# Optimization experiments

Measured on AMD Instinct MI355X. Metric: run time of the kernel, lower is better.

## Reference

```python
import jax, jax.numpy as jnp
import numpy as np

# dims: NL layers, D=d_model, DI=expand*D, F=d_ff, V=vocab, L=S*C seq, R=dt_rank, N=d_state, K=d_conv
NL, D, DI, F, V, L, R, N, K = 2, 256, 512, 1024, 1024, 1024, 16, 16, 4
B, S, C = 2, 128, 8
EPS = 1e-5


def silu(x):
    return x * jax.nn.sigmoid(x)


def batchnorm(x, g, b):  # x: [B,L,D], normalize over (B,L) per channel (training-mode BatchNorm1d)
    m = x.mean((0, 1))
    v = x.var((0, 1))
    return (x - m) * jax.lax.rsqrt(v + EPS) * g + b


def layernorm(x, g, b):
    m = x.mean(-1, keepdims=True)
    v = x.var(-1, keepdims=True)
    return (x - m) * jax.lax.rsqrt(v + EPS) * g + b


def mamba(x, Win, cw, cb, Wx, Wdt, bdt, A_log, Dsk, Wout, bout):
    # x: [B,L,D] -> [B,L,D]; standard Mamba block with selective scan
    Bsz, Lseq, _ = x.shape
    xz = x @ Win                      # [B,L,2*DI]
    xi, z = jnp.split(xz, 2, axis=-1)
    # depthwise causal conv1d, width K
    xp = jnp.pad(xi, ((0, 0), (K - 1, 0), (0, 0)))
    xc = cb + sum(xp[:, k:k + Lseq, :] * cw[:, k] for k in range(K))
    xc = silu(xc)                     # [B,L,DI]
    xdb = xc @ Wx                     # [B,L,R+2N]
    delta = jax.nn.softplus(xdb[..., :R] @ Wdt + bdt)   # [B,L,DI]
    Bm = xdb[..., R:R + N]            # [B,L,N]
    Cm = xdb[..., R + N:]             # [B,L,N]
    A = -jnp.exp(A_log)               # [DI,N]
    dA = jnp.exp(delta[..., None] * A)                       # [B,L,DI,N]
    dBx = delta[..., None] * Bm[:, :, None, :] * xc[..., None]  # [B,L,DI,N]

    def step(h, inp):
        dA_t, dBx_t, C_t = inp
        h = h * dA_t + dBx_t          # [B,DI,N]
        y = jnp.einsum('bdn,bn->bd', h, C_t)
        return h, y

    h0 = jnp.zeros((Bsz, DI, N), x.dtype)
    _, ys = jax.lax.scan(step, h0, (dA.transpose(1, 0, 2, 3), dBx.transpose(1, 0, 2, 3), Cm.transpose(1, 0, 2)))
    y = ys.transpose(1, 0, 2) + Dsk * xc
    y = y * silu(z)
    return y @ Wout + bout


def _forward(input_ids, emb, pos, Win, conv_w, conv_b, Wx, Wdt, bdt, A_log, Dskip, Wout, bout,
             bn_g, bn_b, ln_g, ln_b, ff_w1, ff_b1, ff_w2, ff_b2, final_w, final_b):
    Bsz, Ssz, Csz = input_ids.shape
    Lseq = Ssz * Csz
    # Encoder: token embedding (scaled) + learned positions, flattened to [B, S*C, D]
    x = emb[input_ids].reshape(Bsz, Lseq, D) * jnp.sqrt(jnp.float32(D)) + pos[:Lseq]
    for i in range(NL):
        f = mamba(x, Win[i, 0], conv_w[i, 0], conv_b[i, 0], Wx[i, 0], Wdt[i, 0], bdt[i, 0],
                  A_log[i, 0], Dskip[i, 0], Wout[i, 0], bout[i, 0])
        f = batchnorm(f, bn_g[i, 0], bn_b[i, 0])
        bk = mamba(x[:, ::-1], Win[i, 1], conv_w[i, 1], conv_b[i, 1], Wx[i, 1], Wdt[i, 1], bdt[i, 1],
                   A_log[i, 1], Dskip[i, 1], Wout[i, 1], bout[i, 1])
        bk = batchnorm(bk, bn_g[i, 1], bn_b[i, 1])[:, ::-1]
        f = layernorm(x + f, ln_g[i, 0], ln_b[i, 0])
        bk = layernorm(x + bk, ln_g[i, 1], ln_b[i, 1])
        out = f + bk
        out = jax.nn.relu(out @ ff_w1[i] + ff_b1[i]) @ ff_w2[i] + ff_b2[i]
        out = batchnorm(out, bn_g[i, 2], bn_b[i, 2])
        x = out + x
    return x.reshape(Bsz, Ssz, Csz, D) @ final_w + final_b   # [B,S,C,V]


def setup_inputs() -> dict:
    key = jax.random.key(0)
    ks = list(jax.random.split(key, 16))
    kit = iter(ks)
    rn = lambda shape, s=0.02: jax.random.normal(next(kit), shape, jnp.float32) * s
    inp = {
        'input_ids': jax.random.randint(next(kit), (B, S, C), 0, V),
        'emb': rn((V, D)), 'pos': rn((L, D)),
        'Win': rn((NL, 2, D, 2 * DI)),
        'conv_w': rn((NL, 2, DI, K), 0.1), 'conv_b': jnp.zeros((NL, 2, DI)),
        'Wx': rn((NL, 2, DI, R + 2 * N)),
        'Wdt': rn((NL, 2, R, DI)), 'bdt': jnp.full((NL, 2, DI), -4.0),
        'A_log': jnp.broadcast_to(jnp.log(jnp.arange(1, N + 1, dtype=jnp.float32)), (NL, 2, DI, N)) + 0.0,
        'Dskip': jnp.ones((NL, 2, DI)),
        'Wout': rn((NL, 2, DI, D)), 'bout': jnp.zeros((NL, 2, D)),
        'bn_g': jnp.ones((NL, 3, D)), 'bn_b': jnp.zeros((NL, 3, D)),
        'ln_g': jnp.ones((NL, 2, D)), 'ln_b': jnp.zeros((NL, 2, D)),
        'ff_w1': rn((NL, D, F)), 'ff_b1': jnp.zeros((NL, F)),
        'ff_w2': rn((NL, F, D)), 'ff_b2': jnp.zeros((NL, D)),
        'final_w': rn((D, V)), 'final_b': jnp.zeros((V,)),
    }
    return inp


def reference(input_ids, emb, pos, Win, conv_w, conv_b, Wx, Wdt, bdt, A_log, Dskip, Wout, bout,
              bn_g, bn_b, ln_g, ln_b, ff_w1, ff_b1, ff_w2, ff_b2, final_w, final_b):
    return _forward(input_ids, emb, pos, Win, conv_w, conv_b, Wx, Wdt, bdt, A_log, Dskip, Wout, bout,
                    bn_g, bn_b, ln_g, ln_b, ff_w1, ff_b1, ff_w2, ff_b2, final_w, final_b)
```

## Files before the change

### kernel.cpp

```cpp
#include <hip/hip_runtime.h>

#define NL 2
#define DMODEL 256
#define DI 512
#define FF 1024
#define VV 1024
#define LSEQ 1024
#define RR 16
#define NN 16
#define KCONV 4
#define BTOK 2048
#define EPS 1e-5f

using short8 = __attribute__((ext_vector_type(8))) short;
using float4v = __attribute__((ext_vector_type(4))) float;
typedef unsigned short u16;

__device__ inline float bf2f(u16 u) {
    union { unsigned u; float f; } x; x.u = (unsigned)u << 16; return x.f;
}
__device__ inline u16 f2bf(float f) {
    union { float f; unsigned u; } x; x.f = f;
    unsigned r = x.u + 0x7fffu + ((x.u >> 16) & 1u);
    return (u16)(r >> 16);
}

#if __has_builtin(__builtin_amdgcn_exp2f)
#define EXP2(x) __builtin_amdgcn_exp2f(x)
#else
#define EXP2(x) exp2f(x)
#endif

struct TMat { const float* src; u16* dst; int rows, cols, tile0, tilecols; };
struct TTable { TMat m[24]; int nmat; };

__global__ __launch_bounds__(256) void transpose_kernel(TTable tt) {
    __shared__ u16 tile[32][33];
    int bx = blockIdx.x;
    int j = 0;
    for (int k = 1; k < tt.nmat; ++k) if (bx >= tt.m[k].tile0) j = k;
    TMat mm = tt.m[j];
    int lt = bx - mm.tile0;
    int r0 = (lt / mm.tilecols) * 32, c0 = (lt % mm.tilecols) * 32;
    int tx = threadIdx.x & 31, ty = threadIdx.x >> 5;
    #pragma unroll
    for (int k = 0; k < 4; ++k) {
        int r = r0 + ty + k * 8, c = c0 + tx;
        tile[ty + k * 8][tx] = (r < mm.rows && c < mm.cols) ? f2bf(mm.src[(size_t)r * mm.cols + c]) : (u16)0;
    }
    __syncthreads();
    #pragma unroll
    for (int k = 0; k < 4; ++k) {
        int c = c0 + ty + k * 8, r = r0 + tx;
        if (c < mm.cols && r < mm.rows) mm.dst[(size_t)c * mm.rows + r] = tile[tx][ty + k * 8];
    }
}

__global__ __launch_bounds__(256) void gemm_kernel(
    const u16* __restrict__ A0, int lda, unsigned long long sA,
    const u16* __restrict__ B0, int ldb, unsigned long long sB,
    const float* __restrict__ bias0, unsigned long long sBias,
    void* __restrict__ C0, int ldc, unsigned long long sC,
    int M, int N, int K, int act, int outfp)
{
    const u16* A = A0 + (size_t)blockIdx.z * sA;
    const u16* Bt = B0 + (size_t)blockIdx.z * sB;
    const float* bias = bias0 ? (bias0 + (size_t)blockIdx.z * sBias) : nullptr;

    int tid = threadIdx.x;
    int wv = tid >> 6, lane = tid & 63;
    int row0 = blockIdx.y * 64 + (wv >> 1) * 32;
    int col0 = blockIdx.x * 64 + (wv & 1) * 32;
    int mi = lane & 15, kq = lane >> 4;

    float4v acc[2][2];
    #pragma unroll
    for (int a = 0; a < 2; ++a)
        #pragma unroll
        for (int b = 0; b < 2; ++b) acc[a][b] = (float4v){0.f, 0.f, 0.f, 0.f};
    const short8 zer = {0, 0, 0, 0, 0, 0, 0, 0};

    for (int kk = 0; kk < K; kk += 32) {
        int k = kk + kq * 8;
        bool kv = (k < K);
        short8 af[2], bf[2];
        #pragma unroll
        for (int rt = 0; rt < 2; ++rt) {
            int r = row0 + rt * 16 + mi;
            af[rt] = kv ? *(const short8*)(A + (size_t)r * lda + k) : zer;
        }
        #pragma unroll
        for (int ct = 0; ct < 2; ++ct) {
            int n = col0 + ct * 16 + mi;
            bf[ct] = (kv && n < N) ? *(const short8*)(Bt + (size_t)n * ldb + k) : zer;
        }
        #pragma unroll
        for (int rt = 0; rt < 2; ++rt)
            #pragma unroll
            for (int ct = 0; ct < 2; ++ct)
                acc[rt][ct] = __builtin_amdgcn_mfma_f32_16x16x32_bf16(af[rt], bf[ct], acc[rt][ct], 0, 0, 0);
    }

    #pragma unroll
    for (int rt = 0; rt < 2; ++rt)
        #pragma unroll
        for (int ct = 0; ct < 2; ++ct) {
            int n = col0 + ct * 16 + mi;
            if (n >= N) continue;
            float bv = bias ? bias[n] : 0.f;
            #pragma unroll
            for (int r = 0; r < 4; ++r) {
                int m = row0 + rt * 16 + kq * 4 + r;
                float v = acc[rt][ct][r] + bv;
                if (act == 1) v = fmaxf(v, 0.f);
                if (outfp)
                    ((float*)C0)[(size_t)blockIdx.z * sC + (size_t)m * ldc + n] = v;
                else
                    ((u16*)C0)[(size_t)blockIdx.z * sC + (size_t)m * ldc + n] = f2bf(v);
            }
        }
}

__global__ __launch_bounds__(256) void delta_fused_kernel(
    const u16* __restrict__ xdb, const u16* __restrict__ wdtT,
    const float* __restrict__ bdt, const u16* __restrict__ xc,
    u16* __restrict__ deltaT, u16* __restrict__ uT, int layer)
{
    int z = blockIdx.z;
    const u16* A = xdb + (size_t)z * BTOK * 48;
    const u16* Bt = wdtT + (size_t)z * 512 * 16;
    const float* bias = bdt + (size_t)z * 512;

    int tid = threadIdx.x;
    int wv = tid >> 6, lane = tid & 63;
    int row0 = blockIdx.y * 64 + (wv >> 1) * 32;
    int col0 = blockIdx.x * 64 + (wv & 1) * 32;
    int mi = lane & 15, kq = lane >> 4;

    float4v acc[2][2];
    #pragma unroll
    for (int a = 0; a < 2; ++a)
        #pragma unroll
        for (int b = 0; b < 2; ++b) acc[a][b] = (float4v){0.f, 0.f, 0.f, 0.f};
    const short8 zer = {0, 0, 0, 0, 0, 0, 0, 0};

    int k = kq * 8;
    bool kv = (k < 16);
    short8 af[2], bf[2];
    #pragma unroll
    for (int rt = 0; rt < 2; ++rt) {
        int r = row0 + rt * 16 + mi;
        af[rt] = kv ? *(const short8*)(A + (size_t)r * 48 + k) : zer;
    }
    #pragma unroll
    for (int ct = 0; ct < 2; ++ct) {
        int n = col0 + ct * 16 + mi;
        bf[ct] = kv ? *(const short8*)(Bt + (size_t)n * 16 + k) : zer;
    }
    #pragma unroll
    for (int rt = 0; rt < 2; ++rt)
        #pragma unroll
        for (int ct = 0; ct < 2; ++ct)
            acc[rt][ct] = __builtin_amdgcn_mfma_f32_16x16x32_bf16(af[rt], bf[ct], acc[rt][ct], 0, 0, 0);

    #pragma unroll
    for (int rt = 0; rt < 2; ++rt)
        #pragma unroll
        for (int ct = 0; ct < 2; ++ct) {
            int n = col0 + ct * 16 + mi;
            float bv = bias[n];
            #pragma unroll
            for (int r = 0; r < 4; ++r) {
                int m = row0 + rt * 16 + kq * 4 + r;
                float v = acc[rt][ct][r] + bv;
                v = (v > 20.f) ? v : logf(1.f + __expf(v));
                float xcv = bf2f(xc[((size_t)z * BTOK + m) * DI + n]);
                int b = m >> 10, t = m & 1023;
                size_t off = ((size_t)((z * 2 + b) * DI + n)) * LSEQ + t;
                deltaT[off] = f2bf(v);
                uT[off] = f2bf(v * xcv);
            }
        }
}

__global__ __launch_bounds__(256) void bct_kernel(
    const u16* __restrict__ xdb, u16* __restrict__ bcT)
{
    __shared__ u16 tile[32][34];
    int slab = blockIdx.y;
    int t0 = blockIdx.x * 32;
    int tx = threadIdx.x & 31, ty = threadIdx.x >> 5;
    #pragma unroll
    for (int k = 0; k < 4; ++k) {
        int t = t0 + ty + k * 8;
        tile[tx][ty + k * 8] = xdb[(size_t)(slab * 1024 + t) * 48 + 16 + tx];
    }
    __syncthreads();
    #pragma unroll
    for (int k = 0; k < 4; ++k) {
        int col = ty + k * 8;
        bcT[((size_t)(slab * 32 + col)) * LSEQ + t0 + tx] = tile[col][tx];
    }
}

__global__ __launch_bounds__(256) void embed_kernel(
    const int* __restrict__ ids, const float* __restrict__ emb,
    const float* __restrict__ pos, u16* __restrict__ x)
{
    int tok = blockIdx.x, d = threadIdx.x;
    int id = ids[tok];
    float v = emb[(size_t)id * DMODEL + d] * 16.0f + pos[(size_t)(tok & (LSEQ - 1)) * DMODEL + d];
    x[(size_t)tok * DMODEL + d] = f2bf(v);
}

__global__ __launch_bounds__(256) void conv_kernel(
    const u16* __restrict__ xz, const float* __restrict__ conv_w,
    const float* __restrict__ conv_b, u16* __restrict__ xc, int layer)
{
    unsigned g = blockIdx.x * 256u + threadIdx.x;
    int d = g & 511;
    int t = (g >> 9) & 1023;
    int b = (g >> 19) & 1;
    int dir = g >> 20;
    int wbase = ((layer * 2 + dir) * DI + d);
    float acc = conv_b[wbase];
    int colbase = dir * 1024 + d;
    #pragma unroll
    for (int k = 0; k < KCONV; ++k) {
        int ts = dir ? (t + 3 - k) : (t - 3 + k);
        if (ts >= 0 && ts < LSEQ)
            acc += conv_w[wbase * KCONV + k] * bf2f(xz[(size_t)((b << 10) + ts) * 2048 + colbase]);
    }
    float v = acc / (1.f + __expf(-acc));
    xc[(size_t)(((dir * 2 + b) << 10) + t) * DI + d] = f2bf(v);
}

template<int DIR>
__device__ __forceinline__ void scan_body(
    const u16* __restrict__ deltaT, const u16* __restrict__ uT,
    const u16* __restrict__ bcT, const float* __restrict__ A_log,
    u16* __restrict__ pT, int layer, int slab,
    float* Ps, float* Qs)
{
    const int c = threadIdx.x;
    const int d = blockIdx.x;

    float a2[16];
    const float* al = A_log + (size_t)(((layer * 2 + DIR) * DI + d) * NN);
    #pragma unroll
    for (int n = 0; n < 16; ++n) a2[n] = -__expf(al[n]) * 1.44269504f;

    const size_t tb = ((size_t)(slab * DI + d)) * LSEQ;
    const size_t bcb = (size_t)slab * 32 * LSEQ;
    const int T0 = DIR ? (1016 - 8 * c) : (8 * c);

    short8 dlv = *(const short8*)(deltaT + tb + T0);
    short8 uvv = *(const short8*)(uT + tb + T0);
    float dls[8], uvs[8];
    #pragma unroll
    for (int s = 0; s < 8; ++s) {
        const int idx = DIR ? 7 - s : s;
        dls[s] = bf2f((u16)dlv[idx]);
        uvs[s] = bf2f((u16)uvv[idx]);
    }

    const int base = c * 17;
    #pragma unroll
    for (int n = 0; n < 16; ++n) {
        short8 B8 = *(const short8*)(bcT + bcb + (size_t)n * LSEQ + T0);
        float P = 1.f, Q = 0.f;
        #pragma unroll
        for (int s = 0; s < 8; ++s) {
            const int idx = DIR ? 7 - s : s;
            float dA = EXP2(dls[s] * a2[n]);
            Q = Q * dA + uvs[s] * bf2f((u16)B8[idx]);
            P *= dA;
        }
        Ps[base + n] = P;
        Qs[base + n] = Q;
    }
    __syncthreads();

    for (int off = 1; off < 128; off <<= 1) {
        float np[16], nq[16];
        const bool act = (c >= off);
        if (act) {
            const int nb = (c - off) * 17;
            #pragma unroll
            for (int n = 0; n < 16; ++n) { np[n] = Ps[nb + n]; nq[n] = Qs[nb + n]; }
        }
        __syncthreads();
        if (act) {
            #pragma unroll
            for (int n = 0; n < 16; ++n) {
                float p = Ps[base + n], q = Qs[base + n];
                Qs[base + n] = fmaf(p, nq[n], q);
                Ps[base + n] = p * np[n];
            }
        }
        __syncthreads();
    }

    float pacc[8];
    #pragma unroll
    for (int s = 0; s < 8; ++s) pacc[s] = 0.f;
    const int hb = (c - 1) * 17;
    #pragma unroll
    for (int n = 0; n < 16; ++n) {
        short8 B8 = *(const short8*)(bcT + bcb + (size_t)n * LSEQ + T0);
        short8 C8 = *(const short8*)(bcT + bcb + (size_t)(16 + n) * LSEQ + T0);
        float h = (c == 0) ? 0.f : Qs[hb + n];
        #pragma unroll
        for (int s = 0; s < 8; ++s) {
            const int idx = DIR ? 7 - s : s;
            float dA = EXP2(dls[s] * a2[n]);
            h = h * dA + uvs[s] * bf2f((u16)B8[idx]);
            pacc[s] = fmaf(h, bf2f((u16)C8[idx]), pacc[s]);
        }
    }
    short8 pk;
    #pragma unroll
    for (int s = 0; s < 8; ++s) {
        const int idx = DIR ? 7 - s : s;
        pk[idx] = (short)f2bf(pacc[s]);
    }
    *(short8*)(pT + tb + T0) = pk;
}

__global__ __launch_bounds__(128) void scan_kernel(
    const u16* __restrict__ deltaT, const u16* __restrict__ uT,
    const u16* __restrict__ bcT, const float* __restrict__ A_log,
    u16* __restrict__ pT, int layer)
{
    __shared__ float Ps[128 * 17], Qs[128 * 17];
    int slab = blockIdx.y;
    if (slab >> 1)
        scan_body<1>(deltaT, uT, bcT, A_log, pT, layer, slab, Ps, Qs);
    else
        scan_body<0>(deltaT, uT, bcT, A_log, pT, layer, slab, Ps, Qs);
}

__global__ __launch_bounds__(256) void gate_kernel(
    const u16* __restrict__ pT, const u16* __restrict__ xc,
    const u16* __restrict__ xz, const float* __restrict__ Dskip,
    u16* __restrict__ y, int layer)
{
    __shared__ float tile[32][33];
    int z = blockIdx.z, dir = z >> 1, b = z & 1;
    int d0 = blockIdx.x * 32, t0 = blockIdx.y * 32;
    int tx = threadIdx.x & 31, ty = threadIdx.x >> 5;
    #pragma unroll
    for (int k = 0; k < 4; ++k) {
        int d = d0 + ty + k * 8;
        tile[ty + k * 8][tx] = bf2f(pT[((size_t)(z * DI + d)) * LSEQ + t0 + tx]);
    }
    __syncthreads();
    #pragma unroll
    for (int k = 0; k < 4; ++k) {
        int t = t0 + ty + k * 8, d = d0 + tx;
        float p = tile[tx][ty + k * 8];
        float xcv = bf2f(xc[(size_t)((z << 10) + t) * DI + d]);
        float zv = bf2f(xz[(size_t)((b << 10) + t) * 2048 + dir * 1024 + 512 + d]);
        float dsk = Dskip[(layer * 2 + dir) * DI + d];
        float yv = (p + dsk * xcv) * (zv / (1.f + __expf(-zv)));
        y[(size_t)((z << 10) + t) * DI + d] = f2bf(yv);
    }
}

__global__ __launch_bounds__(256) void bnstats_kernel(
    const u16* __restrict__ p0, const u16* __restrict__ p1, float* __restrict__ stats)
{
    int d = blockIdx.x, arr = blockIdx.y, tid = threadIdx.x;
    const u16* p = arr ? p1 : p0;
    float s = 0.f, q = 0.f;
    #pragma unroll
    for (int k = 0; k < 8; ++k) {
        float v = bf2f(p[(size_t)(tid + k * 256) * DMODEL + d]);
        s += v; q += v * v;
    }
    #pragma unroll
    for (int off = 1; off < 64; off <<= 1) { s += __shfl_xor(s, off); q += __shfl_xor(q, off); }
    __shared__ float ss[4], qs[4];
    if ((tid & 63) == 0) { ss[tid >> 6] = s; qs[tid >> 6] = q; }
    __syncthreads();
    if (tid == 0) {
        float S = ss[0] + ss[1] + ss[2] + ss[3];
        float Q2 = qs[0] + qs[1] + qs[2] + qs[3];
        float mean = S * (1.f / 2048.f);
        float var = Q2 * (1.f / 2048.f) - mean * mean;
        stats[(arr * DMODEL + d) * 2] = mean;
        stats[(arr * DMODEL + d) * 2 + 1] = rsqrtf(var + EPS);
    }
}

__global__ __launch_bounds__(256) void fuseln_kernel(
    const u16* __restrict__ x, const u16* __restrict__ outm, const float* __restrict__ stats,
    const float* __restrict__ bng, const float* __restrict__ bnb,
    const float* __restrict__ lng, const float* __restrict__ lnb, u16* __restrict__ ffin)
{
    int tok = blockIdx.x, d = threadIdx.x;
    float xv = bf2f(x[(size_t)tok * DMODEL + d]);
    float of = bf2f(outm[(size_t)tok * DMODEL + d]);
    float ob = bf2f(outm[(size_t)BTOK * DMODEL + (size_t)tok * DMODEL + d]);
    float vf = xv + (of - stats[d * 2]) * stats[d * 2 + 1] * bng[d] + bnb[d];
    float vb = xv + (ob - stats[(DMODEL + d) * 2]) * stats[(DMODEL + d) * 2 + 1] * bng[DMODEL + d] + bnb[DMODEL + d];
    float s0 = vf, s1 = vf * vf, s2 = vb, s3 = vb * vb;
    #pragma unroll
    for (int off = 1; off < 64; off <<= 1) {
        s0 += __shfl_xor(s0, off); s1 += __shfl_xor(s1, off);
        s2 += __shfl_xor(s2, off); s3 += __shfl_xor(s3, off);
    }
    __shared__ float sm[4][4];
    if ((d & 63) == 0) { sm[d >> 6][0] = s0; sm[d >> 6][1] = s1; sm[d >> 6][2] = s2; sm[d >> 6][3] = s3; }
    __syncthreads();
    s0 = sm[0][0] + sm[1][0] + sm[2][0] + sm[3][0];
    s1 = sm[0][1] + sm[1][1] + sm[2][1] + sm[3][1];
    s2 = sm[0][2] + sm[1][2] + sm[2][2] + sm[3][2];
    s3 = sm[0][3] + sm[1][3] + sm[2][3] + sm[3][3];
    float mf = s0 * (1.f / 256.f), vvf = s1 * (1.f / 256.f) - mf * mf;
    float mb = s2 * (1.f / 256.f), vvb = s3 * (1.f / 256.f) - mb * mb;
    float fl = (vf - mf) * rsqrtf(vvf + EPS) * lng[d] + lnb[d];
    float bl = (vb - mb) * rsqrtf(vvb + EPS) * lng[DMODEL + d] + lnb[DMODEL + d];
    ffin[(size_t)tok * DMODEL + d] = f2bf(fl + bl);
}

__global__ __launch_bounds__(256) void bnadd_kernel(
    u16* __restrict__ x, const u16* __restrict__ ffo, const float* __restrict__ stats,
    const float* __restrict__ g, const float* __restrict__ b)
{
    int tok = blockIdx.x, d = threadIdx.x;
    size_t idx = (size_t)tok * DMODEL + d;
    float v = bf2f(x[idx]) + (bf2f(ffo[idx]) - stats[d * 2]) * stats[d * 2 + 1] * g[d] + b[d];
    x[idx] = f2bf(v);
}

extern "C" void kernel_launch(void* const* d_in, const int* in_sizes, int n_in,
                              void* d_out, int out_size, void* d_ws, size_t ws_size,
                              hipStream_t stream)
{
    const int*   ids     = (const int*)d_in[0];
    const float* emb     = (const float*)d_in[1];
    const float* pos     = (const float*)d_in[2];
    const float* Win     = (const float*)d_in[3];
    const float* conv_w  = (const float*)d_in[4];
    const float* conv_b  = (const float*)d_in[5];
    const float* Wx      = (const float*)d_in[6];
    const float* Wdt     = (const float*)d_in[7];
    const float* bdt     = (const float*)d_in[8];
    const float* A_log   = (const float*)d_in[9];
    const float* Dskip   = (const float*)d_in[10];
    const float* Wout    = (const float*)d_in[11];
    const float* bout    = (const float*)d_in[12];
    const float* bn_g    = (const float*)d_in[13];
    const float* bn_b    = (const float*)d_in[14];
    const float* ln_g    = (const float*)d_in[15];
    const float* ln_b    = (const float*)d_in[16];
    const float* ff_w1   = (const float*)d_in[17];
    const float* ff_b1   = (const float*)d_in[18];
    const float* ff_w2   = (const float*)d_in[19];
    const float* ff_b2   = (const float*)d_in[20];
    const float* final_w = (const float*)d_in[21];
    const float* final_b = (const float*)d_in[22];

    char* cur = (char*)d_ws;
    auto alloc = [&](size_t elems) {
        u16* p = (u16*)cur;
        cur += ((elems * 2 + 511) / 512) * 512;
        return p;
    };
    u16* winT  = alloc((size_t)NL * 2048 * 256);
    u16* wxT   = alloc((size_t)NL * 2 * 48 * 512);
    u16* wdtT  = alloc((size_t)NL * 2 * 512 * 16);
    u16* woutT = alloc((size_t)NL * 2 * 256 * 512);
    u16* fw1T  = alloc((size_t)NL * 1024 * 256);
    u16* fw2T  = alloc((size_t)NL * 256 * 1024);
    u16* finT  = alloc((size_t)1024 * 256);
    u16* xbuf   = alloc((size_t)BTOK * DMODEL);
    u16* xz     = alloc((size_t)BTOK * 2048);
    u16* xc     = alloc((size_t)2 * BTOK * DI);
    u16* xdb    = alloc((size_t)2 * BTOK * 48);
    u16* bcT    = alloc((size_t)4 * 32 * LSEQ);
    u16* deltaT = alloc((size_t)2 * BTOK * DI);
    u16* uT     = alloc((size_t)2 * BTOK * DI);
    u16* pT     = alloc((size_t)2 * BTOK * DI);
    u16* ybuf   = alloc((size_t)2 * BTOK * DI);
    u16* outm   = alloc((size_t)2 * BTOK * DMODEL);
    u16* ffin   = alloc((size_t)BTOK * DMODEL);
    u16* ffh    = alloc((size_t)BTOK * FF);
    u16* ffo    = alloc((size_t)BTOK * DMODEL);
    float* statsM = (float*)alloc(4096);
    float* statsF = statsM + 1024;

    TTable tt; int nm = 0, tiles = 0;
    auto addT = [&](const float* src, u16* dst, int rows, int cols) {
        int tc = (cols + 31) / 32, tr = (rows + 31) / 32;
        tt.m[nm] = {src, dst, rows, cols, tiles, tc};
        tiles += tc * tr; nm++;
    };
    for (int i = 0; i < NL; ++i) {
        for (int dir = 0; dir < 2; ++dir) {
            addT(Win  + (size_t)(i * 2 + dir) * 256 * 1024, winT  + (size_t)i * 2048 * 256 + (size_t)dir * 1024 * 256, 256, 1024);
            addT(Wx   + (size_t)(i * 2 + dir) * 512 * 48,   wxT   + (size_t)(i * 2 + dir) * 48 * 512,   512, 48);
            addT(Wdt  + (size_t)(i * 2 + dir) * 16 * 512,   wdtT  + (size_t)(i * 2 + dir) * 512 * 16,   16, 512);
            addT(Wout + (size_t)(i * 2 + dir) * 512 * 256,  woutT + (size_t)(i * 2 + dir) * 256 * 512,  512, 256);
        }
        addT(ff_w1 + (size_t)i * 256 * 1024, fw1T + (size_t)i * 1024 * 256, 256, 1024);
        addT(ff_w2 + (size_t)i * 1024 * 256, fw2T + (size_t)i * 256 * 1024, 1024, 256);
    }
    addT(final_w, finT, 256, 1024);
    tt.nmat = nm;
    transpose_kernel<<<tiles, 256, 0, stream>>>(tt);

    embed_kernel<<<BTOK, 256, 0, stream>>>(ids, emb, pos, xbuf);

    auto gemm = [&](const u16* A, int lda, size_t sA, const u16* Bt, int ldb, size_t sB,
                    const float* bias, size_t sBias, void* C, int ldc, size_t sC,
                    int M, int N, int K, int act, int nb, int outfp) {
        dim3 g((N + 63) / 64, M / 64, nb);
        gemm_kernel<<<g, 256, 0, stream>>>(A, lda, (unsigned long long)sA, Bt, ldb, (unsigned long long)sB,
                                           bias, (unsigned long long)sBias, C, ldc, (unsigned long long)sC,
                                           M, N, K, act, outfp);
    };

    for (int i = 0; i < NL; ++i) {
        gemm(xbuf, 256, 0, winT + (size_t)i * 2048 * 256, 256, 0, nullptr, 0,
             xz, 2048, 0, BTOK, 2048, 256, 0, 1, 0);
        conv_kernel<<<(2 * BTOK * DI) / 256, 256, 0, stream>>>(xz, conv_w, conv_b, xc, i);
        gemm(xc, 512, (size_t)BTOK * 512, wxT + (size_t)i * 2 * 48 * 512, 512, 48 * 512,
             nullptr, 0, xdb, 48, (size_t)BTOK * 48, BTOK, 48, 512, 0, 2, 0);
        bct_kernel<<<dim3(32, 4), 256, 0, stream>>>(xdb, bcT);
        delta_fused_kernel<<<dim3(8, 32, 2), 256, 0, stream>>>(
            xdb, wdtT + (size_t)i * 2 * 512 * 16, bdt + (size_t)i * 2 * 512, xc, deltaT, uT, i);
        scan_kernel<<<dim3(512, 4), 128, 0, stream>>>(deltaT, uT, bcT, A_log, pT, i);
        gate_kernel<<<dim3(DI / 32, LSEQ / 32, 4), 256, 0, stream>>>(pT, xc, xz, Dskip, ybuf, i);
        gemm(ybuf, 512, (size_t)BTOK * 512, woutT + (size_t)i * 2 * 256 * 512, 512, 256 * 512,
             bout + (size_t)i * 2 * 256, 256, outm, 256, (size_t)BTOK * 256, BTOK, 256, 512, 0, 2, 0);
        bnstats_kernel<<<dim3(256, 2), 256, 0, stream>>>(outm, outm + (size_t)BTOK * 256, statsM);
        fuseln_kernel<<<BTOK, 256, 0, stream>>>(xbuf, outm, statsM,
            bn_g + (size_t)i * 3 * 256, bn_b + (size_t)i * 3 * 256,
            ln_g + (size_t)i * 2 * 256, ln_b + (size_t)i * 2 * 256, ffin);
        gemm(ffin, 256, 0, fw1T + (size_t)i * 1024 * 256, 256, 0,
             ff_b1 + (size_t)i * 1024, 0, ffh, 1024, 0, BTOK, 1024, 256, 1, 1, 0);
        gemm(ffh, 1024, 0, fw2T + (size_t)i * 256 * 1024, 1024, 0,
             ff_b2 + (size_t)i * 256, 0, ffo, 256, 0, BTOK, 256, 1024, 0, 1, 0);
        bnstats_kernel<<<dim3(256, 1), 256, 0, stream>>>(ffo, ffo, statsF);
        bnadd_kernel<<<BTOK, 256, 0, stream>>>(xbuf, ffo, statsF,
            bn_g + (size_t)(i * 3 + 2) * 256, bn_b + (size_t)(i * 3 + 2) * 256);
    }
    gemm(xbuf, 256, 0, finT, 256, 0, final_b, 0,
         d_out, 1024, 0, BTOK, 1024, 256, 0, 1, 1);
}
```

Baseline: 433.6 us.

## Add LDS-staged MFMA GEMM with larger tiles for the big projections

Adds a templated GEMM that stages A and B tiles into LDS with global_load_lds direct loads and computes larger per-block tiles (128x128 or 128x64) using 16x16x32 bf16 MFMA. The in-projection, FFN, out-projection and final head GEMMs move to it, while the small x-projection keeps the old kernel. The aim is more operand reuse per block and fewer global loads than the old 64x64 tile kernel. It is single-buffered with syncthreads around each K step and assumes dimensions divisible by the tiles.

```diff
diff --git a/kernel.cpp b/kernel.cpp
--- a/kernel.cpp
+++ b/kernel.cpp
@@ -54,6 +54,81 @@
         int c = c0 + ty + k * 8, r = r0 + tx;
         if (c < mm.cols && r < mm.rows) mm.dst[(size_t)c * mm.rows + r] = tile[tx][ty + k * 8];
     }
+}
+
+template<int BN, int WR, int WC, int RT, int CT>
+__global__ __launch_bounds__(256) void sgemm_kernel(
+    const u16* __restrict__ A0, int lda, unsigned long long sA,
+    const u16* __restrict__ B0, int ldb, unsigned long long sB,
+    const float* __restrict__ bias0, unsigned long long sBias,
+    void* __restrict__ C0, int ldc, unsigned long long sC,
+    int K, int act, int outfp)
+{
+    constexpr int BM = 128, BK = 32;
+    __shared__ u16 As[BM * BK];
+    __shared__ u16 Bs[BN * BK];
+    const u16* A = A0 + (size_t)blockIdx.z * sA;
+    const u16* Bt = B0 + (size_t)blockIdx.z * sB;
+    const float* bias = bias0 ? (bias0 + (size_t)blockIdx.z * sBias) : nullptr;
+
+    const int tid = threadIdx.x, w = tid >> 6, lane = tid & 63;
+    const int row0 = blockIdx.y * BM, col0 = blockIdx.x * BN;
+    const int wr = w / WC, wc = w % WC;
+    const int mi = lane & 15, kq = lane >> 4;
+    const int lr = lane >> 2, lc = (lane & 3) * 8;
+
+    float4v acc[RT][CT];
+    #pragma unroll
+    for (int i = 0; i < RT; ++i)
+        #pragma unroll
+        for (int j = 0; j < CT; ++j) acc[i][j] = (float4v){0.f, 0.f, 0.f, 0.f};
+
+    for (int kk = 0; kk < K; kk += BK) {
+        __syncthreads();
+        for (int i = w; i < BM / 16; i += 4) {
+            const u16* g = A + (size_t)(row0 + i * 16 + lr) * lda + kk + lc;
+            __builtin_amdgcn_global_load_lds(
+                (const __attribute__((address_space(1))) void*)g,
+                (__attribute__((address_space(3))) void*)(As + i * 16 * BK), 16, 0, 0);
+        }
+        for (int i = w; i < BN / 16; i += 4) {
+            const u16* g = Bt + (size_t)(col0 + i * 16 + lr) * ldb + kk + lc;
+            __builtin_amdgcn_global_load_lds(
+                (const __attribute__((address_space(1))) void*)g,
+                (__attribute__((address_space(3))) void*)(Bs + i * 16 * BK), 16, 0, 0);
+        }
+        __syncthreads();
+        short8 af[RT], bf[CT];
+        #pragma unroll
+        for (int i = 0; i < RT; ++i)
+            af[i] = *(const short8*)(As + (wr * RT * 16 + i * 16 + mi) * BK + kq * 8);
+        #pragma unroll
+        for (int j = 0; j < CT; ++j)
+            bf[j] = *(const short8*)(Bs + (wc * CT * 16 + j * 16 + mi) * BK + kq * 8);
+        #pragma unroll
+        for (int i = 0; i < RT; ++i)
+            #pragma unroll
+            for (int j = 0; j < CT; ++j)
+                acc[i][j] = __builtin_amdgcn_mfma_f32_16x16x32_bf16(af[i], bf[j], acc[i][j], 0, 0, 0);
+    }
+
+    #pragma unroll
+    for (int i = 0; i < RT; ++i)
+        #pragma unroll
+        for (int j = 0; j < CT; ++j) {
+            int n = col0 + wc * CT * 16 + j * 16 + mi;
+            float bv = bias ? bias[n] : 0.f;
+            #pragma unroll
+            for (int r = 0; r < 4; ++r) {
+                int m = row0 + wr * RT * 16 + i * 16 + kq * 4 + r;
+                float v = acc[i][j][r] + bv;
+                if (act == 1) v = fmaxf(v, 0.f);
+                if (outfp)
+                    ((float*)C0)[(size_t)blockIdx.z * sC + (size_t)m * ldc + n] = v;
+                else
+                    ((u16*)C0)[(size_t)blockIdx.z * sC + (size_t)m * ldc + n] = f2bf(v);
+            }
+        }
 }
 
 __global__ __launch_bounds__(256) void gemm_kernel(
@@ -521,10 +596,26 @@
                                            bias, (unsigned long long)sBias, C, ldc, (unsigned long long)sC,
                                            M, N, K, act, outfp);
     };
+    auto sgemm128 = [&](const u16* A, int lda, const u16* Bt, int ldb, size_t sB,
+                        const float* bias, size_t sBias, void* C, int ldc,
+                        int N, int K, int act, int nb, int outfp) {
+        dim3 g(N / 128, BTOK / 128, nb);
+        sgemm_kernel<128, 2, 2, 4, 4><<<g, 256, 0, stream>>>(
+            A, lda, 0ULL, Bt, ldb, (unsigned long long)sB, bias, (unsigned long long)sBias,
+            C, ldc, 0ULL, K, act, outfp);
+    };
+    auto sgemm64 = [&](const u16* A, int lda, size_t sA, const u16* Bt, int ldb, size_t sB,
+                       const float* bias, size_t sBias, void* C, int ldc, size_t sC,
+                       int N, int K, int act, int nb, int outfp) {
+        dim3 g(N / 64, BTOK / 128, nb);
+        sgemm_kernel<64, 4, 1, 2, 4><<<g, 256, 0, stream>>>(
+            A, lda, (unsigned long long)sA, Bt, ldb, (unsigned long long)sB,
+            bias, (unsigned long long)sBias, C, ldc, (unsigned long long)sC, K, act, outfp);
+    };
 
     for (int i = 0; i < NL; ++i) {
-        gemm(xbuf, 256, 0, winT + (size_t)i * 2048 * 256, 256, 0, nullptr, 0,
-             xz, 2048, 0, BTOK, 2048, 256, 0, 1, 0);
+        sgemm128(xbuf, 256, winT + (size_t)i * 2048 * 256, 256, 0, nullptr, 0,
+                 xz, 2048, 2048, 256, 0, 1, 0);
         conv_kernel<<<(2 * BTOK * DI) / 256, 256, 0, stream>>>(xz, conv_w, conv_b, xc, i);
         gemm(xc, 512, (size_t)BTOK * 512, wxT + (size_t)i * 2 * 48 * 512, 512, 48 * 512,
              nullptr, 0, xdb, 48, (size_t)BTOK * 48, BTOK, 48, 512, 0, 2, 0);
@@ -533,20 +624,20 @@
             xdb, wdtT + (size_t)i * 2 * 512 * 16, bdt + (size_t)i * 2 * 512, xc, deltaT, uT, i);
         scan_kernel<<<dim3(512, 4), 128, 0, stream>>>(deltaT, uT, bcT, A_log, pT, i);
         gate_kernel<<<dim3(DI / 32, LSEQ / 32, 4), 256, 0, stream>>>(pT, xc, xz, Dskip, ybuf, i);
-        gemm(ybuf, 512, (size_t)BTOK * 512, woutT + (size_t)i * 2 * 256 * 512, 512, 256 * 512,
-             bout + (size_t)i * 2 * 256, 256, outm, 256, (size_t)BTOK * 256, BTOK, 256, 512, 0, 2, 0);
+        sgemm64(ybuf, 512, (size_t)BTOK * 512, woutT + (size_t)i * 2 * 256 * 512, 512, 256 * 512,
+                bout + (size_t)i * 2 * 256, 256, outm, 256, (size_t)BTOK * 256, 256, 512, 0, 2, 0);
         bnstats_kernel<<<dim3(256, 2), 256, 0, stream>>>(outm, outm + (size_t)BTOK * 256, statsM);
         fuseln_kernel<<<BTOK, 256, 0, stream>>>(xbuf, outm, statsM,
             bn_g + (size_t)i * 3 * 256, bn_b + (size_t)i * 3 * 256,
             ln_g + (size_t)i * 2 * 256, ln_b + (size_t)i * 2 * 256, ffin);
-        gemm(ffin, 256, 0, fw1T + (size_t)i * 1024 * 256, 256, 0,
-             ff_b1 + (size_t)i * 1024, 0, ffh, 1024, 0, BTOK, 1024, 256, 1, 1, 0);
-        gemm(ffh, 1024, 0, fw2T + (size_t)i * 256 * 1024, 1024, 0,
-             ff_b2 + (size_t)i * 256, 0, ffo, 256, 0, BTOK, 256, 1024, 0, 1, 0);
+        sgemm128(ffin, 256, fw1T + (size_t)i * 1024 * 256, 256, 0,
+                 ff_b1 + (size_t)i * 1024, 0, ffh, 1024, 1024, 256, 1, 1, 0);
+        sgemm64(ffh, 1024, 0, fw2T + (size_t)i * 256 * 1024, 1024, 0,
+                ff_b2 + (size_t)i * 256, 0, ffo, 256, 0, 256, 1024, 0, 1, 0);
         bnstats_kernel<<<dim3(256, 1), 256, 0, stream>>>(ffo, ffo, statsF);
         bnadd_kernel<<<BTOK, 256, 0, stream>>>(xbuf, ffo, statsF,
             bn_g + (size_t)(i * 3 + 2) * 256, bn_b + (size_t)(i * 3 + 2) * 256);
     }
-    gemm(xbuf, 256, 0, finT, 256, 0, final_b, 0,
-         d_out, 1024, 0, BTOK, 1024, 256, 0, 1, 1);
-}
+    sgemm128(xbuf, 256, finT, 256, 0, final_b, 0,
+             d_out, 1024, 1024, 256, 0, 1, 1);
+}
```

Result: no change. 434.8 us (+0.3%).
